# Kernel tuning notes

Hardware: AMD Instinct MI355X
Metric: run time of the kernel (lower is better)

Reference implementation:

```python
import jax, jax.numpy as jnp
import numpy as np

EPSILON = 1.5  # quality-tolerance threshold from init_kwargs
NEG_INF = -1000000000.0


def setup_inputs() -> dict:
    key = jax.random.key(0)
    k1, k2, k3 = jax.random.split(key, 3)
    B, S, D, E = 4, 4096, 2048, 64
    return {
        "hidden_states": jax.random.normal(k1, (B, S, D), dtype=jnp.float32),
        "gate_W": jax.random.normal(k2, (E, D), dtype=jnp.float32),  # nn.Linear weight [out,in]
        "secret_projection": jax.random.normal(k3, (D, E), dtype=jnp.float32),
        "top_k": 2,
    }


def reference(hidden_states, gate_W, secret_projection, top_k):
    # raw gate logits: Linear without bias -> x @ W^T
    raw_logits = jnp.einsum("bsd,ed->bse", hidden_states, gate_W)
    # watermark bias via secret LSH projection
    watermark_bias = jnp.einsum("bsd,de->bse", hidden_states, secret_projection)
    # indifference zone: experts whose logit is within epsilon of the max
    max_logits = jnp.max(raw_logits, axis=-1, keepdims=True)
    safe_mask = raw_logits >= max_logits - EPSILON
    modified_scores = jnp.where(safe_mask, watermark_bias, jnp.asarray(NEG_INF, raw_logits.dtype))
    # top-k over watermark-preferred safe experts
    _, selected_experts = jax.lax.top_k(modified_scores, top_k)
    # gather original logits at selected experts, softmax over the k slots
    router_logits = jnp.take_along_axis(raw_logits, selected_experts, axis=-1)
    routing_weights = jax.nn.softmax(router_logits, axis=-1)
    return routing_weights, selected_experts
```

## Files before the change

kernel.cpp:

```cpp
#include <hip/hip_runtime.h>
#include <stdint.h>


#define DDIM 2048
#define NEXP 64
#define TOKB 64
#define KSPL 4
#define NTS  16
#define NEG_INF  -1000000000.0f
#define MRG_RAW  0.04f
#define MRG_WM   0.15f

typedef __attribute__((ext_vector_type(8))) short bf16x8;
typedef __attribute__((ext_vector_type(4))) float f32x4;

union BFrag { bf16x8 v; f32x4 f; uint32_t w[4]; uint4 q; };

__device__ inline void split8_rne(const float* a, bf16x8* hi, bf16x8* lo) {
    BFrag h, l;
    #pragma unroll
    for (int p = 0; p < 4; ++p) {
        const uint32_t u0 = __float_as_uint(a[2*p]);
        const uint32_t u1 = __float_as_uint(a[2*p+1]);
        const uint32_t h0 = (u0 + 0x7FFFu + ((u0 >> 16) & 1u)) >> 16;
        const uint32_t h1 = (u1 + 0x7FFFu + ((u1 >> 16) & 1u)) >> 16;
        const float r0 = a[2*p]   - __uint_as_float(h0 << 16);
        const float r1 = a[2*p+1] - __uint_as_float(h1 << 16);
        const uint32_t v0 = __float_as_uint(r0);
        const uint32_t v1 = __float_as_uint(r1);
        const uint32_t l0 = (v0 + 0x7FFFu + ((v0 >> 16) & 1u)) >> 16;
        const uint32_t l1 = (v1 + 0x7FFFu + ((v1 >> 16) & 1u)) >> 16;
        h.w[p] = h0 | (h1 << 16);
        l.w[p] = l0 | (l1 << 16);
    }
    *hi = h.v; *lo = l.v;
}

__device__ inline void split8t(const float* a, bf16x8* hi, bf16x8* lo) {
    BFrag h, l;
    #pragma unroll
    for (int p = 0; p < 4; ++p) {
        const uint32_t u0 = __float_as_uint(a[2*p]);
        const uint32_t u1 = __float_as_uint(a[2*p+1]);
        h.w[p] = (u0 >> 16) | (u1 & 0xFFFF0000u);
        const float r0 = a[2*p]   - __uint_as_float(u0 & 0xFFFF0000u);
        const float r1 = a[2*p+1] - __uint_as_float(u1 & 0xFFFF0000u);
        l.w[p] = (__float_as_uint(r0) >> 16) | (__float_as_uint(r1) & 0xFFFF0000u);
    }
    *hi = h.v; *lo = l.v;
}

__global__ void prep_b(const float* __restrict__ gateW, const float* __restrict__ secret,
                       uint4* __restrict__ wsB) {
    const int kstep = blockIdx.x;
    const int s = threadIdx.x >> 6;
    const int l = threadIdx.x & 63;
    const int col = s * 16 + (l & 15);
    const int kb  = kstep * 32 + (l >> 4) * 8;
    float v[8];
    if (col < NEXP) {
        #pragma unroll
        for (int j = 0; j < 8; ++j) v[j] = gateW[(size_t)col * DDIM + kb + j];
    } else {
        #pragma unroll
        for (int j = 0; j < 8; ++j) v[j] = secret[(size_t)(kb + j) * NEXP + (col - NEXP)];
    }
    bf16x8 hi, lo; split8_rne(v, &hi, &lo);
    const size_t base = (size_t)(kstep * 8 + s) * 128 + l;
    BFrag t;
    t.v = hi; wsB[base]      = t.q;
    t.v = lo; wsB[base + 64] = t.q;
}

__device__ inline void gl_lds16(const char* g, char* l) {
    __builtin_amdgcn_global_load_lds(
        (const __attribute__((address_space(1))) void*)g,
        (__attribute__((address_space(3))) void*)l, 16, 0, 0);
}

__device__ inline f32x4 ds128(unsigned addr) {
    f32x4 r;
    asm volatile("ds_read_b128 %0, %1" : "=v"(r) : "v"(addr));
    return r;
}

__global__ __launch_bounds__(256, 3)
void gemm_c(const float* __restrict__ x, const char* __restrict__ wsB,
            float* __restrict__ wsP, int ntok)
{
    __shared__ __align__(16) char lds[2][24576];

    const int tid = threadIdx.x;
    const int w = tid >> 6, l = tid & 63;
    const int c = l & 15;
    const int g = l >> 4;
    const int q  = blockIdx.x & (KSPL - 1);
    const int mb = blockIdx.x / KSPL;
    const int rowbase = mb * TOKB;
    const int wrow = rowbase + w * 16;

    f32x4 acc[8];
    #pragma unroll
    for (int s = 0; s < 8; ++s) acc[s] = (f32x4){0.f, 0.f, 0.f, 0.f};

    const char*  bq = wsB + (size_t)(q * NTS) * 16384;
    const float* xq = x + q * (DDIM / KSPL);

    #define STAGE(ts, buf)                                                         \
        {                                                                          \
            _Pragma("unroll")                                                      \
            for (int j = 0; j < 4; ++j) {                                          \
                const int slot = j * 256 + tid;                                    \
                gl_lds16(bq + (size_t)(ts) * 16384 + slot * 16,                    \
                         &lds[buf][slot * 16]);                                    \
            }                                                                      \
            _Pragma("unroll")                                                      \
            for (int j = 0; j < 2; ++j) {                                          \
                const int a = j * 256 + tid;                                       \
                const int r = a >> 3, cg = a & 7;                                  \
                const int scg = cg ^ (r & 7);                                      \
                gl_lds16((const char*)(xq + (size_t)(rowbase + r) * DDIM           \
                                       + (ts) * 32 + scg * 4),                     \
                         &lds[buf][16384 + a * 16]);                               \
            }                                                                      \
        }

    STAGE(0, 0);

    #pragma unroll 1
    for (int ts = 0; ts < NTS; ++ts) {
        const int cur = ts & 1;
        if (ts + 1 < NTS) {
            STAGE(ts + 1, cur ^ 1);
            asm volatile("s_waitcnt vmcnt(6)" ::: "memory");
        } else {
            asm volatile("s_waitcnt vmcnt(0)" ::: "memory");
        }
        __builtin_amdgcn_s_barrier();

        const unsigned bb = (unsigned)(size_t)&lds[cur][0];

        const int r = w * 16 + c;
        const unsigned arow = bb + 16384u + (unsigned)(r * 128);
        BFrag fa, fb;
        fa.f = ds128(arow + (unsigned)((( 2 * g)     ^ (r & 7)) * 16));
        fb.f = ds128(arow + (unsigned)(((2 * g + 1) ^ (r & 7)) * 16));
        BFrag bf[16];
        #pragma unroll
        for (int i = 0; i < 16; ++i)
            bf[i].f = ds128(bb + (unsigned)(i * 1024 + l * 16));

        asm volatile("s_waitcnt lgkmcnt(0)" ::: "memory");
        __builtin_amdgcn_sched_barrier(0);

        const float va[8] = {fa.f[0], fa.f[1], fa.f[2], fa.f[3],
                             fb.f[0], fb.f[1], fb.f[2], fb.f[3]};
        bf16x8 ah, al;
        split8t(va, &ah, &al);

        __builtin_amdgcn_s_setprio(1);
        #pragma unroll
        for (int s = 0; s < 8; ++s) {
            acc[s] = __builtin_amdgcn_mfma_f32_16x16x32_bf16(ah, bf[2*s].v,     acc[s], 0, 0, 0);
            acc[s] = __builtin_amdgcn_mfma_f32_16x16x32_bf16(ah, bf[2*s + 1].v, acc[s], 0, 0, 0);
            acc[s] = __builtin_amdgcn_mfma_f32_16x16x32_bf16(al, bf[2*s].v,     acc[s], 0, 0, 0);
        }
        __builtin_amdgcn_s_setprio(0);

        __builtin_amdgcn_s_barrier();
    }
    #undef STAGE

    const size_t MN = (size_t)ntok * 128;
    #pragma unroll
    for (int s = 0; s < 8; ++s)
        #pragma unroll
        for (int r = 0; r < 4; ++r)
            wsP[(size_t)q * MN + (size_t)(wrow + g * 4 + r) * 128 + s * 16 + c] = acc[s][r];
}

template <int KSPLIT>
__global__ __launch_bounds__(256, 4)
void router_k(const float* __restrict__ wsP,
              const float* __restrict__ x,
              const float* __restrict__ gateW,
              const float* __restrict__ secret,
              float* __restrict__ out, int ntok)
{
    const int t = blockIdx.x * 4 + (threadIdx.x >> 6);
    const int e = threadIdx.x & 63;
    const size_t MN = (size_t)ntok * 128;

    float raw = 0.f, wm = 0.f;
    #pragma unroll
    for (int q = 0; q < KSPLIT; ++q) {
        raw += wsP[(size_t)q * MN + (size_t)t * 128 + e];
        wm  += wsP[(size_t)q * MN + (size_t)t * 128 + NEXP + e];
    }

    float rmax = raw;
    #pragma unroll
    for (int off = 32; off; off >>= 1) rmax = fmaxf(rmax, __shfl_xor(rmax, off));

    if (__any(fabsf(raw - (rmax - 1.5f)) < MRG_RAW)) {
        float s0 = 0.f, s1 = 0.f, s2 = 0.f, s3 = 0.f;
        const float4* xr = reinterpret_cast<const float4*>(x + (size_t)t * DDIM);
        const float4* wr = reinterpret_cast<const float4*>(gateW + (size_t)e * DDIM);
        for (int k = 0; k < DDIM / 4; ++k) {
            const float4 a = xr[k], b = wr[k];
            s0 = fmaf(a.x, b.x, s0); s1 = fmaf(a.y, b.y, s1);
            s2 = fmaf(a.z, b.z, s2); s3 = fmaf(a.w, b.w, s3);
        }
        raw = (s0 + s1) + (s2 + s3);
        rmax = raw;
        #pragma unroll
        for (int off = 32; off; off >>= 1) rmax = fmaxf(rmax, __shfl_xor(rmax, off));
    }

    const bool safe = (raw >= rmax - 1.5f);
    float m = safe ? wm : NEG_INF;

    float v1 = m; int e1 = e;
    #pragma unroll
    for (int off = 32; off; off >>= 1) {
        const float ov = __shfl_xor(v1, off); const int oi = __shfl_xor(e1, off);
        if (ov > v1 || (ov == v1 && oi < e1)) { v1 = ov; e1 = oi; }
    }
    float v2 = (e == e1) ? -3.0e38f : m; int e2 = e;
    #pragma unroll
    for (int off = 32; off; off >>= 1) {
        const float ov = __shfl_xor(v2, off); const int oi = __shfl_xor(e2, off);
        if (ov > v2 || (ov == v2 && oi < e2)) { v2 = ov; e2 = oi; }
    }
    float v3 = (e == e1 || e == e2) ? -3.0e38f : m; int e3 = e;
    #pragma unroll
    for (int off = 32; off; off >>= 1) {
        const float ov = __shfl_xor(v3, off); const int oi = __shfl_xor(e3, off);
        if (ov > v3 || (ov == v3 && oi < e3)) { v3 = ov; e3 = oi; }
    }

    const bool wmRisk = (v2 > NEG_INF + 1.0f && v1 - v2 < MRG_WM) ||
                        (v3 > NEG_INF + 1.0f && v2 - v3 < MRG_WM);
    if (__any(wmRisk)) {
        float s0 = 0.f, s1 = 0.f, s2 = 0.f, s3 = 0.f;
        const float* xr = x + (size_t)t * DDIM;
        for (int k = 0; k < DDIM; k += 4) {
            s0 = fmaf(xr[k + 0], secret[(size_t)(k + 0) * NEXP + e], s0);
            s1 = fmaf(xr[k + 1], secret[(size_t)(k + 1) * NEXP + e], s1);
            s2 = fmaf(xr[k + 2], secret[(size_t)(k + 2) * NEXP + e], s2);
            s3 = fmaf(xr[k + 3], secret[(size_t)(k + 3) * NEXP + e], s3);
        }
        m = safe ? ((s0 + s1) + (s2 + s3)) : NEG_INF;
        v1 = m; e1 = e;
        #pragma unroll
        for (int off = 32; off; off >>= 1) {
            const float ov = __shfl_xor(v1, off); const int oi = __shfl_xor(e1, off);
            if (ov > v1 || (ov == v1 && oi < e1)) { v1 = ov; e1 = oi; }
        }
        v2 = (e == e1) ? -3.0e38f : m; e2 = e;
        #pragma unroll
        for (int off = 32; off; off >>= 1) {
            const float ov = __shfl_xor(v2, off); const int oi = __shfl_xor(e2, off);
            if (ov > v2 || (ov == v2 && oi < e2)) { v2 = ov; e2 = oi; }
        }
    }

    const float l1 = __shfl(raw, e1);
    const float l2 = __shfl(raw, e2);

    if (e == 0) {
        const float mm = fmaxf(l1, l2);
        const float x1 = expf(l1 - mm), x2 = expf(l2 - mm);
        const float inv = 1.0f / (x1 + x2);
        out[(size_t)t * 2 + 0] = x1 * inv;
        out[(size_t)t * 2 + 1] = x2 * inv;
        out[(size_t)2 * ntok + t * 2 + 0] = (float)e1;
        out[(size_t)2 * ntok + t * 2 + 1] = (float)e2;
    }
}

extern "C" void kernel_launch(void* const* d_in, const int* in_sizes, int n_in,
                              void* d_out, int out_size, void* d_ws, size_t ws_size,
                              hipStream_t stream) {
    const float* x      = (const float*)d_in[0];
    const float* gateW  = (const float*)d_in[1];
    const float* secret = (const float*)d_in[2];
    float* out = (float*)d_out;

    const int ntok = in_sizes[0] / DDIM;
    uint4* wsB = (uint4*)d_ws;
    float* wsP = (float*)((char*)d_ws + (2u << 20));

    prep_b<<<64, 512, 0, stream>>>(gateW, secret, wsB);
    gemm_c<<<(ntok / TOKB) * KSPL, 256, 0, stream>>>(x, (const char*)wsB, wsP, ntok);
    router_k<KSPL><<<ntok / 4, 256, 0, stream>>>(wsP, x, gateW, secret, out, ntok);
}
```

Before: 99.40 us.

## Load activation tile directly to registers and split B LDS reads into halves

The activation rows no longer go through LDS. Each lane loads its own 8 floats straight from global memory into registers, prefetched two k-steps ahead in a fully unrolled loop, and LDS holds only the B fragments. LDS per block drops from 48 KB to 32 KB and launch bounds go from 3 to 4 blocks per CU for higher occupancy. B fragments are read in two halves of 8 to cut register pressure. The cost is uncoalesced-ish per-lane strided global loads of x and a large unrolled prefetch register array.

```diff
diff --git a/kernel.cpp b/kernel.cpp
--- a/kernel.cpp
+++ b/kernel.cpp
@@ -84,11 +84,11 @@
     return r;
 }
 
-__global__ __launch_bounds__(256, 3)
-void gemm_c(const float* __restrict__ x, const char* __restrict__ wsB,
+__global__ __launch_bounds__(256, 4)
+void gemm_d(const float* __restrict__ x, const char* __restrict__ wsB,
             float* __restrict__ wsP, int ntok)
 {
-    __shared__ __align__(16) char lds[2][24576];
+    __shared__ __align__(16) char lds[2][16384];
 
     const int tid = threadIdx.x;
     const int w = tid >> 6, l = tid & 63;
@@ -96,17 +96,16 @@
     const int g = l >> 4;
     const int q  = blockIdx.x & (KSPL - 1);
     const int mb = blockIdx.x / KSPL;
-    const int rowbase = mb * TOKB;
-    const int wrow = rowbase + w * 16;
+    const int wrow = mb * TOKB + w * 16;
 
     f32x4 acc[8];
     #pragma unroll
     for (int s = 0; s < 8; ++s) acc[s] = (f32x4){0.f, 0.f, 0.f, 0.f};
 
     const char*  bq = wsB + (size_t)(q * NTS) * 16384;
-    const float* xq = x + q * (DDIM / KSPL);
-
-    #define STAGE(ts, buf)                                                         \
+    const float* xr = x + (size_t)(wrow + c) * DDIM + q * (DDIM / KSPL) + g * 8;
+
+    #define STAGE_B(ts, buf)                                                       \
         {                                                                          \
             _Pragma("unroll")                                                      \
             for (int j = 0; j < 4; ++j) {                                          \
@@ -114,62 +113,67 @@
                 gl_lds16(bq + (size_t)(ts) * 16384 + slot * 16,                    \
                          &lds[buf][slot * 16]);                                    \
             }                                                                      \
-            _Pragma("unroll")                                                      \
-            for (int j = 0; j < 2; ++j) {                                          \
-                const int a = j * 256 + tid;                                       \
-                const int r = a >> 3, cg = a & 7;                                  \
-                const int scg = cg ^ (r & 7);                                      \
-                gl_lds16((const char*)(xq + (size_t)(rowbase + r) * DDIM           \
-                                       + (ts) * 32 + scg * 4),                     \
-                         &lds[buf][16384 + a * 16]);                               \
-            }                                                                      \
-        }
-
-    STAGE(0, 0);
-
-    #pragma unroll 1
+        }
+    #define TSC(t) ((t) < NTS ? (t) : NTS - 1)
+
+    float4 Aa[NTS + 2], Ab[NTS + 2];
+
+    STAGE_B(0, 0);
+    Aa[0] = *reinterpret_cast<const float4*>(xr);
+    Ab[0] = *reinterpret_cast<const float4*>(xr + 4);
+    Aa[1] = *reinterpret_cast<const float4*>(xr + 32);
+    Ab[1] = *reinterpret_cast<const float4*>(xr + 36);
+
+    #pragma unroll
     for (int ts = 0; ts < NTS; ++ts) {
-        const int cur = ts & 1;
-        if (ts + 1 < NTS) {
-            STAGE(ts + 1, cur ^ 1);
-            asm volatile("s_waitcnt vmcnt(6)" ::: "memory");
-        } else {
-            asm volatile("s_waitcnt vmcnt(0)" ::: "memory");
-        }
+        STAGE_B(TSC(ts + 1), (ts + 1) & 1);
+        Aa[ts + 2] = *reinterpret_cast<const float4*>(xr + TSC(ts + 2) * 32);
+        Ab[ts + 2] = *reinterpret_cast<const float4*>(xr + TSC(ts + 2) * 32 + 4);
+
+        asm volatile("s_waitcnt vmcnt(8)" ::: "memory");
         __builtin_amdgcn_s_barrier();
 
-        const unsigned bb = (unsigned)(size_t)&lds[cur][0];
-
-        const int r = w * 16 + c;
-        const unsigned arow = bb + 16384u + (unsigned)(r * 128);
-        BFrag fa, fb;
-        fa.f = ds128(arow + (unsigned)((( 2 * g)     ^ (r & 7)) * 16));
-        fb.f = ds128(arow + (unsigned)(((2 * g + 1) ^ (r & 7)) * 16));
-        BFrag bf[16];
-        #pragma unroll
-        for (int i = 0; i < 16; ++i)
+        const unsigned bb = (unsigned)(size_t)&lds[ts & 1][0];
+
+        const float va[8] = {Aa[ts].x, Aa[ts].y, Aa[ts].z, Aa[ts].w,
+                             Ab[ts].x, Ab[ts].y, Ab[ts].z, Ab[ts].w};
+        bf16x8 ah, al;
+        split8t(va, &ah, &al);
+
+        BFrag bf[8];
+        #pragma unroll
+        for (int i = 0; i < 8; ++i)
             bf[i].f = ds128(bb + (unsigned)(i * 1024 + l * 16));
-
         asm volatile("s_waitcnt lgkmcnt(0)" ::: "memory");
         __builtin_amdgcn_sched_barrier(0);
-
-        const float va[8] = {fa.f[0], fa.f[1], fa.f[2], fa.f[3],
-                             fb.f[0], fb.f[1], fb.f[2], fb.f[3]};
-        bf16x8 ah, al;
-        split8t(va, &ah, &al);
-
         __builtin_amdgcn_s_setprio(1);
         #pragma unroll
-        for (int s = 0; s < 8; ++s) {
+        for (int s = 0; s < 4; ++s) {
             acc[s] = __builtin_amdgcn_mfma_f32_16x16x32_bf16(ah, bf[2*s].v,     acc[s], 0, 0, 0);
             acc[s] = __builtin_amdgcn_mfma_f32_16x16x32_bf16(ah, bf[2*s + 1].v, acc[s], 0, 0, 0);
             acc[s] = __builtin_amdgcn_mfma_f32_16x16x32_bf16(al, bf[2*s].v,     acc[s], 0, 0, 0);
         }
         __builtin_amdgcn_s_setprio(0);
 
+        #pragma unroll
+        for (int i = 0; i < 8; ++i)
+            bf[i].f = ds128(bb + (unsigned)((8 + i) * 1024 + l * 16));
+        asm volatile("s_waitcnt lgkmcnt(0)" ::: "memory");
+        __builtin_amdgcn_sched_barrier(0);
+        __builtin_amdgcn_s_setprio(1);
+        #pragma unroll
+        for (int s = 4; s < 8; ++s) {
+            const int i = s - 4;
+            acc[s] = __builtin_amdgcn_mfma_f32_16x16x32_bf16(ah, bf[2*i].v,     acc[s], 0, 0, 0);
+            acc[s] = __builtin_amdgcn_mfma_f32_16x16x32_bf16(ah, bf[2*i + 1].v, acc[s], 0, 0, 0);
+            acc[s] = __builtin_amdgcn_mfma_f32_16x16x32_bf16(al, bf[2*i].v,     acc[s], 0, 0, 0);
+        }
+        __builtin_amdgcn_s_setprio(0);
+
         __builtin_amdgcn_s_barrier();
     }
-    #undef STAGE
+    #undef STAGE_B
+    #undef TSC
 
     const size_t MN = (size_t)ntok * 128;
     #pragma unroll
@@ -292,6 +296,6 @@
     float* wsP = (float*)((char*)d_ws + (2u << 20));
 
     prep_b<<<64, 512, 0, stream>>>(gateW, secret, wsB);
-    gemm_c<<<(ntok / TOKB) * KSPL, 256, 0, stream>>>(x, (const char*)wsB, wsP, ntok);
+    gemm_d<<<(ntok / TOKB) * KSPL, 256, 0, stream>>>(x, (const char*)wsB, wsP, ntok);
     router_k<KSPL><<<ntok / 4, 256, 0, stream>>>(wsP, x, gateW, secret, out, ntok);
 }
```

Result: no change. 100.7 us (+1.3%).
